# Kernel optimization log

Hardware: AMD Instinct MI355X
Metric: run time of the kernel (lower is better)

## Reference

```python
import jax, jax.numpy as jnp
import numpy as np

GAMMA = 1.0  # kernel_gamma

def setup_inputs() -> dict:
    key = jax.random.key(0)
    ks = jax.random.split(key, 8)
    B, T, D, P, H = 32, 512, 256, 512, 512
    return {
        "x": jax.random.normal(ks[0], (B, T, D), dtype=jnp.float32),
        "prototypes": jax.random.normal(ks[1], (P, D), dtype=jnp.float32),
        "W_lin": jax.random.normal(ks[2], (H, P), dtype=jnp.float32) * (1.0 / np.sqrt(P)),
        "b_lin": jax.random.normal(ks[3], (H,), dtype=jnp.float32) * 0.01,
        "W_ih": jax.random.normal(ks[4], (4 * H, H), dtype=jnp.float32) * (1.0 / np.sqrt(H)),
        "W_hh": jax.random.normal(ks[5], (4 * H, H), dtype=jnp.float32) * (1.0 / np.sqrt(H)),
        "b_ih": jax.random.normal(ks[6], (4 * H,), dtype=jnp.float32) * 0.01,
        "b_hh": jax.random.normal(ks[7], (4 * H,), dtype=jnp.float32) * 0.01,
    }

def _rbf(x_flat, prototypes):
    x2 = jnp.sum(x_flat * x_flat, axis=-1, keepdims=True)          # (N, 1)
    p2 = jnp.sum(prototypes * prototypes, axis=-1)                  # (P,)
    sq = x2 + p2[None, :] - 2.0 * (x_flat @ prototypes.T)           # (N, P)
    return jnp.exp(-GAMMA * jnp.maximum(sq, 0.0))

def _lstm(feats, W_ih, W_hh, b_ih, b_hh):
    # feats: (B, T, H); torch gate order i, f, g, o; zero initial state
    B, T, H = feats.shape
    xs = jnp.einsum('bth,gh->tbg', feats, W_ih) + (b_ih + b_hh)     # (T, B, 4H)

    def step(carry, x_t):
        h, c = carry
        gates = x_t + h @ W_hh.T                                     # (B, 4H)
        i, f, g, o = jnp.split(gates, 4, axis=-1)
        i, f, o = jax.nn.sigmoid(i), jax.nn.sigmoid(f), jax.nn.sigmoid(o)
        g = jnp.tanh(g)
        c = f * c + i * g
        h = o * jnp.tanh(c)
        return (h, c), h

    h0 = jnp.zeros((B, H), dtype=feats.dtype)
    c0 = jnp.zeros((B, H), dtype=feats.dtype)
    _, hs = jax.lax.scan(step, (h0, c0), xs)                         # hs: (T, B, H)
    return jnp.transpose(hs, (1, 0, 2))                              # (B, T, H)

def reference(x, prototypes, W_lin, b_lin, W_ih, W_hh, b_ih, b_hh):
    B, T, D = x.shape
    feats = _rbf(x.reshape(B * T, D), prototypes)                    # (B*T, P)
    feats = feats.reshape(B, T, -1) @ W_lin.T + b_lin                # (B, T, H)
    return _lstm(feats, W_ih, W_hh, b_ih, b_hh)
```

## Files before the change

kernel.cpp:

```cpp
#include <hip/hip_runtime.h>

#define Bb 32
#define Tt 512
#define Dd 256
#define Pp 512
#define Hh 512
#define G4 2048
#define TC 128
#define NG 8
#define WPG 16
#define NBG 4

__device__ __forceinline__ float sigmf(float x){ return 1.0f/(1.0f+__expf(-x)); }
__device__ __forceinline__ float tanhf_(float x){ return 1.0f - 2.0f/(__expf(2.0f*x)+1.0f); }

typedef __attribute__((ext_vector_type(8))) short v8s;
typedef __attribute__((ext_vector_type(4))) float f32x4;

__global__ void k_rowsq(const float* __restrict__ A, float* __restrict__ o, int M, int K){
  int m = blockIdx.x*blockDim.x + threadIdx.x;
  if (m >= M) return;
  const float4* a4 = (const float4*)(A + (size_t)m*K);
  float s = 0.f;
  for (int i = 0; i < K/4; ++i){ float4 v = a4[i]; s += v.x*v.x + v.y*v.y + v.z*v.z + v.w*v.w; }
  o[m] = s;
}

__global__ void k_transpose(const float* __restrict__ in, float* __restrict__ out, int M, int N){
  __shared__ float tile[32][33];
  int bn = blockIdx.x * 32;
  int bm = blockIdx.y * 32;
  int tx = threadIdx.x, ty = threadIdx.y;
  #pragma unroll
  for (int i = 0; i < 32; i += 8)
    tile[ty+i][tx] = in[(size_t)(bm+ty+i)*N + bn+tx];
  __syncthreads();
  #pragma unroll
  for (int i = 0; i < 32; i += 8)
    out[(size_t)(bn+ty+i)*M + bm+tx] = tile[tx][ty+i];
}

__global__ void k_bx(const float* __restrict__ Wih, const float* __restrict__ blin,
                     const float* __restrict__ bih, const float* __restrict__ bhh,
                     float* __restrict__ bx){
  int r = blockIdx.x*blockDim.x + threadIdx.x;
  const float4* w4 = (const float4*)(Wih + (size_t)r*Hh);
  const float4* b4 = (const float4*)blin;
  float s = 0.f;
  for (int i = 0; i < Hh/4; ++i){ float4 w=w4[i], b=b4[i]; s += w.x*b.x+w.y*b.y+w.z*b.z+w.w*b.w; }
  bx[r] = s + bih[r] + bhh[r];
}

__global__ void k_cvt_bf16(const float* __restrict__ in, ushort* __restrict__ out, int n4){
  int i = blockIdx.x*blockDim.x + threadIdx.x;
  if (i >= n4) return;
  float4 v = ((const float4*)in)[i];
  ushort4 o;
  uint u;
  u = __float_as_uint(v.x); u += 0x7FFF + ((u>>16)&1); o.x = (ushort)(u>>16);
  u = __float_as_uint(v.y); u += 0x7FFF + ((u>>16)&1); o.y = (ushort)(u>>16);
  u = __float_as_uint(v.z); u += 0x7FFF + ((u>>16)&1); o.z = (ushort)(u>>16);
  u = __float_as_uint(v.w); u += 0x7FFF + ((u>>16)&1); o.w = (ushort)(u>>16);
  ((ushort4*)out)[i] = o;
}

template<int EPI, bool REMAP>
__global__ __launch_bounds__(256) void k_gemm(const float* __restrict__ A, const float* __restrict__ Bm,
                                              float* __restrict__ C, int M, int N, int K,
                                              const float* __restrict__ rowAux,
                                              const float* __restrict__ colAux, int t0)
{
  __shared__ float As[16][132];
  __shared__ float Bs[16][68];
  const int tid = threadIdx.x;
  const int bm = blockIdx.x * 128;
  const int bn = blockIdx.y * 64;
  const int tm = (tid & 15) * 8;
  const int tn = (tid >> 4) * 4;
  const int arow = tid >> 1;
  const int akq  = (tid & 1) * 8;
  const int brow = tid >> 4;
  const int bcol = (tid & 15) * 4;
  const int am = bm + arow;
  const size_t aRow = REMAP ? ((size_t)(am >> 7) * Tt + t0 + (am & 127)) : (size_t)am;
  float acc[8][4] = {};
  for (int k0 = 0; k0 < K; k0 += 16){
    float4 a0 = *(const float4*)&A[aRow*K + k0 + akq];
    float4 a1 = *(const float4*)&A[aRow*K + k0 + akq + 4];
    float4 bv = *(const float4*)&Bm[(size_t)(k0 + brow)*N + bn + bcol];
    As[akq+0][arow]=a0.x; As[akq+1][arow]=a0.y; As[akq+2][arow]=a0.z; As[akq+3][arow]=a0.w;
    As[akq+4][arow]=a1.x; As[akq+5][arow]=a1.y; As[akq+6][arow]=a1.z; As[akq+7][arow]=a1.w;
    *(float4*)&Bs[brow][bcol] = bv;
    __syncthreads();
    #pragma unroll
    for (int kk = 0; kk < 16; ++kk){
      float4 x0 = *(const float4*)&As[kk][tm];
      float4 x1 = *(const float4*)&As[kk][tm+4];
      float4 y  = *(const float4*)&Bs[kk][tn];
      float av[8] = {x0.x,x0.y,x0.z,x0.w,x1.x,x1.y,x1.z,x1.w};
      #pragma unroll
      for (int i=0;i<8;++i){
        float a = av[i];
        acc[i][0] += a*y.x; acc[i][1] += a*y.y; acc[i][2] += a*y.z; acc[i][3] += a*y.w;
      }
    }
    __syncthreads();
  }
  #pragma unroll
  for (int i=0;i<8;++i){
    int m = bm + tm + i;
    size_t mAux = REMAP ? ((size_t)(m >> 7) * Tt + t0 + (m & 127)) : (size_t)m;
    float4 o;
    float vv[4];
    #pragma unroll
    for (int j=0;j<4;++j){
      int n = bn + tn + j;
      float v = acc[i][j];
      if (EPI==1) v = __expf(-fmaxf(rowAux[mAux] + colAux[n] - 2.f*v, 0.f));
      vv[j] = v;
    }
    o.x=vv[0]; o.y=vv[1]; o.z=vv[2]; o.w=vv[3];
    *(float4*)&C[(size_t)m*N + bn + tn] = o;
  }
}

__global__ __launch_bounds__(256) void k_xs_mfma(
    const ushort* __restrict__ A, const ushort* __restrict__ Bm,
    const float* __restrict__ bx, float* __restrict__ C, int M, int N, int K)
{
  __shared__ ushort As[128][72];
  __shared__ ushort Ws[128][72];
  const int tid  = threadIdx.x;
  const int bm   = blockIdx.x * 128;
  const int bn   = blockIdx.y * 128;
  const int lane = tid & 63;
  const int w    = tid >> 6;
  const int wr   = w >> 1, wc = w & 1;
  const int srow = tid >> 1;
  const int scol = (tid & 1) * 32;
  const int fr   = lane & 15;
  const int fk   = (lane >> 4) * 8;

  f32x4 acc[4][4] = {};

  for (int k0 = 0; k0 < K; k0 += 64){
    const ushort* ag = &A [(size_t)(bm + srow)*K + k0 + scol];
    const ushort* wg = &Bm[(size_t)(bn + srow)*K + k0 + scol];
    #pragma unroll
    for (int q = 0; q < 4; ++q){
      *(v8s*)&As[srow][scol + q*8] = *(const v8s*)&ag[q*8];
      *(v8s*)&Ws[srow][scol + q*8] = *(const v8s*)&wg[q*8];
    }
    __syncthreads();
    #pragma unroll
    for (int kk = 0; kk < 64; kk += 32){
      v8s af[4], bf[4];
      #pragma unroll
      for (int mi = 0; mi < 4; ++mi)
        af[mi] = *(const v8s*)&As[wr*64 + mi*16 + fr][kk + fk];
      #pragma unroll
      for (int ni = 0; ni < 4; ++ni)
        bf[ni] = *(const v8s*)&Ws[wc*64 + ni*16 + fr][kk + fk];
      #pragma unroll
      for (int mi = 0; mi < 4; ++mi)
        #pragma unroll
        for (int ni = 0; ni < 4; ++ni)
          acc[mi][ni] = __builtin_amdgcn_mfma_f32_16x16x32_bf16(af[mi], bf[ni], acc[mi][ni], 0, 0, 0);
    }
    __syncthreads();
  }

  const int cr = lane >> 4;
  #pragma unroll
  for (int ni = 0; ni < 4; ++ni){
    const int n = bn + wc*64 + ni*16 + fr;
    const float bb = bx[n];
    #pragma unroll
    for (int mi = 0; mi < 4; ++mi){
      #pragma unroll
      for (int r = 0; r < 4; ++r){
        const int m = bm + wr*64 + mi*16 + cr*4 + r;
        C[(size_t)m*N + n] = acc[mi][ni][r] + bb;
      }
    }
  }
}

__global__ __launch_bounds__(512, 2) void k_lstm_persist(
    const float* __restrict__ Whh, const float* __restrict__ xs,
    float* __restrict__ cbuf, float* __restrict__ out, int t0)
{
  __shared__ float hbuf[NBG*Hh];
  const int tid  = threadIdx.x;
  const int gid  = blockIdx.x & 7;
  const int wg   = blockIdx.x >> 3;
  const int gsel = tid & 3;
  const int ks   = (tid >> 2) & 15;
  const int ug   = tid >> 6;
  const int jbase = wg*32 + ug*4;

  float W[4][32];
  #pragma unroll
  for (int r = 0; r < 4; ++r){
    const float* wrow = &Whh[(size_t)(gsel*Hh + jbase + r)*Hh + ks*32];
    #pragma unroll
    for (int c = 0; c < 8; ++c){
      float4 w = *(const float4*)&wrow[c*4];
      W[r][c*4+0]=w.x; W[r][c*4+1]=w.y; W[r][c*4+2]=w.z; W[r][c*4+3]=w.w;
    }
  }

  const int rr = ks >> 2;
  const int bl = ks & 3;
  const int j  = jbase + rr;
  const int b  = gid*NBG + bl;
  float c_st = (t0 == 0) ? 0.f : cbuf[(size_t)b*Hh + j];

  const int sbl = tid >> 7;
  const int skb = (tid & 127) * 4;
  const int ssw = skb ^ (((skb >> 5) & 7) << 2);

  for (int tl = 0; tl < TC; ++tl){
    const int t = t0 + tl;
    float4 hv = {0.f,0.f,0.f,0.f};
    if (t > 0){
      const unsigned long long* src =
        (const unsigned long long*)&out[((size_t)(gid*NBG + sbl)*Tt + (t-1))*Hh + skb];
      unsigned long long a, c;
      for (;;){
        a = __hip_atomic_load(src+0, __ATOMIC_RELAXED, __HIP_MEMORY_SCOPE_AGENT);
        c = __hip_atomic_load(src+1, __ATOMIC_RELAXED, __HIP_MEMORY_SCOPE_AGENT);
        if ((unsigned)a != 0xFFFFFFFFu && (unsigned)(a>>32) != 0xFFFFFFFFu &&
            (unsigned)c != 0xFFFFFFFFu && (unsigned)(c>>32) != 0xFFFFFFFFu) break;
        __builtin_amdgcn_s_sleep(1);
      }
      hv.x = __uint_as_float((unsigned)a);
      hv.y = __uint_as_float((unsigned)(a>>32));
      hv.z = __uint_as_float((unsigned)c);
      hv.w = __uint_as_float((unsigned)(c>>32));
    }
    *(float4*)&hbuf[sbl*Hh + ssw] = hv;
    __syncthreads();

    float acc[4][4];
    #pragma unroll
    for (int r=0;r<4;++r){ acc[r][0]=0.f; acc[r][1]=0.f; acc[r][2]=0.f; acc[r][3]=0.f; }
    #pragma unroll
    for (int blq = 0; blq < 4; ++blq){
      const float* hb = &hbuf[blq*Hh + ks*32];
      #pragma unroll
      for (int c = 0; c < 8; ++c){
        float4 h4 = *(const float4*)&hb[(c*4) ^ ((ks & 7) << 2)];
        #pragma unroll
        for (int r = 0; r < 4; ++r){
          acc[r][blq] = fmaf(W[r][c*4+0], h4.x, acc[r][blq]);
          acc[r][blq] = fmaf(W[r][c*4+1], h4.y, acc[r][blq]);
          acc[r][blq] = fmaf(W[r][c*4+2], h4.z, acc[r][blq]);
          acc[r][blq] = fmaf(W[r][c*4+3], h4.w, acc[r][blq]);
        }
      }
    }

    #pragma unroll
    for (int m = 4; m <= 32; m <<= 1){
      #pragma unroll
      for (int r=0;r<4;++r){
        #pragma unroll
        for (int q=0;q<4;++q)
          acc[r][q] += __shfl_xor(acc[r][q], m, 64);
      }
    }
    float g = acc[0][0];
    #pragma unroll
    for (int r=0;r<4;++r){
      #pragma unroll
      for (int q=0;q<4;++q)
        if (ks == r*4+q) g = acc[r][q];
    }

    g += xs[((size_t)b*TC + tl)*G4 + gsel*Hh + j];
    const int lbase = (tid & 63) & ~3;
    float gi = __shfl(g, lbase+0, 64);
    float gf = __shfl(g, lbase+1, 64);
    float gg = __shfl(g, lbase+2, 64);
    float go = __shfl(g, lbase+3, 64);
    gi = sigmf(gi); gf = sigmf(gf); gg = tanhf_(gg); go = sigmf(go);
    c_st = gf*c_st + gi*gg;
    float h = go * tanhf_(c_st);
    if (gsel == 0)
      __hip_atomic_store(&out[((size_t)b*Tt + t)*Hh + j], h,
                         __ATOMIC_RELAXED, __HIP_MEMORY_SCOPE_AGENT);
  }
  if (gsel == 0) cbuf[(size_t)b*Hh + j] = c_st;
}

extern "C" void kernel_launch(void* const* d_in, const int* in_sizes, int n_in,
                              void* d_out, int out_size, void* d_ws, size_t ws_size,
                              hipStream_t stream)
{
  const float* x    = (const float*)d_in[0];
  const float* prot = (const float*)d_in[1];
  const float* Wlin = (const float*)d_in[2];
  const float* blin = (const float*)d_in[3];
  const float* Wih  = (const float*)d_in[4];
  const float* Whh  = (const float*)d_in[5];
  const float* bih  = (const float*)d_in[6];
  const float* bhh  = (const float*)d_in[7];
  float* out = (float*)d_out;
  float* ws  = (float*)d_ws;

  size_t off = 0;
  auto alloc = [&](size_t n)->float*{ float* p = ws + off; off += (n + 15) & ~((size_t)15); return p; };
  float* x2     = alloc((size_t)Bb*Tt);
  float* p2     = alloc(Pp);
  float* pT     = alloc((size_t)Dd*Pp);
  float* bx     = alloc(G4);
  float* Wx     = alloc((size_t)G4*Pp);
  ushort* WxB   = (ushort*)alloc((size_t)G4*Pp/2);
  float* cbuf   = alloc((size_t)Bb*Hh);
  float* featsC = alloc((size_t)Bb*TC*Pp);
  ushort* featsB= (ushort*)alloc((size_t)Bb*TC*Pp/2);
  float* xsC    = alloc((size_t)Bb*TC*G4);

  hipMemsetAsync(out, 0xFF, (size_t)Bb*Tt*Hh*sizeof(float), stream);

  k_rowsq<<<dim3((Bb*Tt)/256), dim3(256), 0, stream>>>(x, x2, Bb*Tt, Dd);
  k_rowsq<<<dim3(Pp/256), dim3(256), 0, stream>>>(prot, p2, Pp, Dd);
  k_transpose<<<dim3(Dd/32, Pp/32), dim3(32,8), 0, stream>>>(prot, pT, Pp, Dd);
  k_bx<<<dim3(G4/256), dim3(256), 0, stream>>>(Wih, blin, bih, bhh, bx);
  k_gemm<0,false><<<dim3(G4/128, Pp/64), dim3(256), 0, stream>>>(Wih, Wlin, Wx, G4, Pp, Hh, nullptr, nullptr, 0);
  k_cvt_bf16<<<dim3((G4*Pp/4)/256), dim3(256), 0, stream>>>(Wx, WxB, G4*Pp/4);

  for (int ch = 0; ch < Tt/TC; ++ch){
    int t0 = ch * TC;
    k_gemm<1,true><<<dim3((Bb*TC)/128, Pp/64), dim3(256), 0, stream>>>(
        x, pT, featsC, Bb*TC, Pp, Dd, x2, p2, t0);
    k_cvt_bf16<<<dim3((Bb*TC*Pp/4)/256), dim3(256), 0, stream>>>(featsC, featsB, Bb*TC*Pp/4);
    k_xs_mfma<<<dim3((Bb*TC)/128, G4/128), dim3(256), 0, stream>>>(
        featsB, WxB, bx, xsC, Bb*TC, G4, Pp);
    void* args[] = { (void*)&Whh, (void*)&xsC, (void*)&cbuf, (void*)&out, (void*)&t0 };
    hipLaunchCooperativeKernel((void*)k_lstm_persist, dim3(NG*WPG), dim3(512), args, 0, stream);
  }
}
```

Baseline: 3.432 ms.

## Repartition persistent LSTM kernel to one batch per workgroup with 1024 threads

```diff
diff --git a/kernel.cpp b/kernel.cpp
--- a/kernel.cpp
+++ b/kernel.cpp
@@ -7,9 +7,8 @@
 #define Hh 512
 #define G4 2048
 #define TC 128
-#define NG 8
-#define WPG 16
-#define NBG 4
+#define NG 32
+#define WPG 4
 
 __device__ __forceinline__ float sigmf(float x){ return 1.0f/(1.0f+__expf(-x)); }
 __device__ __forceinline__ float tanhf_(float x){ return 1.0f - 2.0f/(__expf(2.0f*x)+1.0f); }
@@ -186,22 +185,24 @@
   }
 }
 
-__global__ __launch_bounds__(512, 2) void k_lstm_persist(
-    const float* __restrict__ Whh, const float* __restrict__ xs,
-    float* __restrict__ cbuf, float* __restrict__ out, int t0)
+__global__ __launch_bounds__(1024) __attribute__((amdgpu_waves_per_eu(4, 4)))
+void k_lstm_persist(const float* __restrict__ Whh, const float* __restrict__ xs,
+                    float* __restrict__ cbuf, float* __restrict__ out, int t0)
 {
-  __shared__ float hbuf[NBG*Hh];
+  __shared__ float hbuf[Hh];
   const int tid  = threadIdx.x;
-  const int gid  = blockIdx.x & 7;
-  const int wg   = blockIdx.x >> 3;
+  const int lane = tid & 63;
   const int gsel = tid & 3;
   const int ks   = (tid >> 2) & 15;
   const int ug   = tid >> 6;
-  const int jbase = wg*32 + ug*4;
-
-  float W[4][32];
-  #pragma unroll
-  for (int r = 0; r < 4; ++r){
+  const int gid  = blockIdx.x & 31;
+  const int wg   = blockIdx.x >> 5;
+  const int jbase = wg*128 + ug*8;
+  const int b    = gid;
+
+  float W[8][32];
+  #pragma unroll
+  for (int r = 0; r < 8; ++r){
     const float* wrow = &Whh[(size_t)(gsel*Hh + jbase + r)*Hh + ks*32];
     #pragma unroll
     for (int c = 0; c < 8; ++c){
@@ -210,53 +211,52 @@
     }
   }
 
-  const int rr = ks >> 2;
-  const int bl = ks & 3;
-  const int j  = jbase + rr;
-  const int b  = gid*NBG + bl;
-  float c_st = (t0 == 0) ? 0.f : cbuf[(size_t)b*Hh + j];
-
-  const int sbl = tid >> 7;
+  const int jown = jbase + (ks & 7);
+  float c_st = (t0 == 0) ? 0.f : cbuf[(size_t)b*Hh + jown];
+
   const int skb = (tid & 127) * 4;
   const int ssw = skb ^ (((skb >> 5) & 7) << 2);
+  const bool stager = (tid < 128);
 
   for (int tl = 0; tl < TC; ++tl){
     const int t = t0 + tl;
-    float4 hv = {0.f,0.f,0.f,0.f};
-    if (t > 0){
-      const unsigned long long* src =
-        (const unsigned long long*)&out[((size_t)(gid*NBG + sbl)*Tt + (t-1))*Hh + skb];
-      unsigned long long a, c;
-      for (;;){
-        a = __hip_atomic_load(src+0, __ATOMIC_RELAXED, __HIP_MEMORY_SCOPE_AGENT);
-        c = __hip_atomic_load(src+1, __ATOMIC_RELAXED, __HIP_MEMORY_SCOPE_AGENT);
-        if ((unsigned)a != 0xFFFFFFFFu && (unsigned)(a>>32) != 0xFFFFFFFFu &&
-            (unsigned)c != 0xFFFFFFFFu && (unsigned)(c>>32) != 0xFFFFFFFFu) break;
-        __builtin_amdgcn_s_sleep(1);
+
+    if (stager){
+      float4 hv = {0.f,0.f,0.f,0.f};
+      if (t > 0){
+        const unsigned long long* src =
+          (const unsigned long long*)&out[((size_t)b*Tt + (t-1))*Hh + skb];
+        unsigned long long a, c;
+        for (;;){
+          a = __hip_atomic_load(src+0, __ATOMIC_RELAXED, __HIP_MEMORY_SCOPE_AGENT);
+          c = __hip_atomic_load(src+1, __ATOMIC_RELAXED, __HIP_MEMORY_SCOPE_AGENT);
+          if ((unsigned)a != 0xFFFFFFFFu && (unsigned)(a>>32) != 0xFFFFFFFFu &&
+              (unsigned)c != 0xFFFFFFFFu && (unsigned)(c>>32) != 0xFFFFFFFFu) break;
+          __builtin_amdgcn_s_sleep(1);
+        }
+        hv.x = __uint_as_float((unsigned)a);
+        hv.y = __uint_as_float((unsigned)(a>>32));
+        hv.z = __uint_as_float((unsigned)c);
+        hv.w = __uint_as_float((unsigned)(c>>32));
       }
-      hv.x = __uint_as_float((unsigned)a);
-      hv.y = __uint_as_float((unsigned)(a>>32));
-      hv.z = __uint_as_float((unsigned)c);
-      hv.w = __uint_as_float((unsigned)(c>>32));
-    }
-    *(float4*)&hbuf[sbl*Hh + ssw] = hv;
-    __syncthreads();
-
-    float acc[4][4];
-    #pragma unroll
-    for (int r=0;r<4;++r){ acc[r][0]=0.f; acc[r][1]=0.f; acc[r][2]=0.f; acc[r][3]=0.f; }
-    #pragma unroll
-    for (int blq = 0; blq < 4; ++blq){
-      const float* hb = &hbuf[blq*Hh + ks*32];
+      *(float4*)&hbuf[ssw] = hv;
+    }
+    __syncthreads();
+
+    float acc[8];
+    #pragma unroll
+    for (int r=0;r<8;++r) acc[r]=0.f;
+    {
+      const float* hb = &hbuf[ks*32];
       #pragma unroll
       for (int c = 0; c < 8; ++c){
         float4 h4 = *(const float4*)&hb[(c*4) ^ ((ks & 7) << 2)];
         #pragma unroll
-        for (int r = 0; r < 4; ++r){
-          acc[r][blq] = fmaf(W[r][c*4+0], h4.x, acc[r][blq]);
-          acc[r][blq] = fmaf(W[r][c*4+1], h4.y, acc[r][blq]);
-          acc[r][blq] = fmaf(W[r][c*4+2], h4.z, acc[r][blq]);
-          acc[r][blq] = fmaf(W[r][c*4+3], h4.w, acc[r][blq]);
+        for (int r = 0; r < 8; ++r){
+          acc[r] = fmaf(W[r][c*4+0], h4.x, acc[r]);
+          acc[r] = fmaf(W[r][c*4+1], h4.y, acc[r]);
+          acc[r] = fmaf(W[r][c*4+2], h4.z, acc[r]);
+          acc[r] = fmaf(W[r][c*4+3], h4.w, acc[r]);
         }
       }
     }
@@ -264,22 +264,16 @@
     #pragma unroll
     for (int m = 4; m <= 32; m <<= 1){
       #pragma unroll
-      for (int r=0;r<4;++r){
-        #pragma unroll
-        for (int q=0;q<4;++q)
-          acc[r][q] += __shfl_xor(acc[r][q], m, 64);
-      }
-    }
-    float g = acc[0][0];
-    #pragma unroll
-    for (int r=0;r<4;++r){
-      #pragma unroll
-      for (int q=0;q<4;++q)
-        if (ks == r*4+q) g = acc[r][q];
-    }
-
-    g += xs[((size_t)b*TC + tl)*G4 + gsel*Hh + j];
-    const int lbase = (tid & 63) & ~3;
+      for (int r=0;r<8;++r)
+        acc[r] += __shfl_xor(acc[r], m, 64);
+    }
+    float g = acc[0];
+    #pragma unroll
+    for (int r=1;r<8;++r)
+      if (ks == r) g = acc[r];
+
+    g += xs[((size_t)b*TC + tl)*G4 + gsel*Hh + jown];
+    const int lbase = lane & ~3;
     float gi = __shfl(g, lbase+0, 64);
     float gf = __shfl(g, lbase+1, 64);
     float gg = __shfl(g, lbase+2, 64);
@@ -287,11 +281,11 @@
     gi = sigmf(gi); gf = sigmf(gf); gg = tanhf_(gg); go = sigmf(go);
     c_st = gf*c_st + gi*gg;
     float h = go * tanhf_(c_st);
-    if (gsel == 0)
-      __hip_atomic_store(&out[((size_t)b*Tt + t)*Hh + j], h,
+    if (gsel == 0 && ks < 8)
+      __hip_atomic_store(&out[((size_t)b*Tt + t)*Hh + jown], h,
                          __ATOMIC_RELAXED, __HIP_MEMORY_SCOPE_AGENT);
   }
-  if (gsel == 0) cbuf[(size_t)b*Hh + j] = c_st;
+  if (gsel == 0 && ks < 8) cbuf[(size_t)b*Hh + jown] = c_st;
 }
 
 extern "C" void kernel_launch(void* const* d_in, const int* in_sizes, int n_in,
@@ -339,6 +333,6 @@
     k_xs_mfma<<<dim3((Bb*TC)/128, G4/128), dim3(256), 0, stream>>>(
         featsB, WxB, bx, xsC, Bb*TC, G4, Pp);
     void* args[] = { (void*)&Whh, (void*)&xsC, (void*)&cbuf, (void*)&out, (void*)&t0 };
-    hipLaunchCooperativeKernel((void*)k_lstm_persist, dim3(NG*WPG), dim3(512), args, 0, stream);
-  }
-}
+    hipLaunchCooperativeKernel((void*)k_lstm_persist, dim3(NG*WPG), dim3(1024), args, 0, stream);
+  }
+}
```

Result: slower. 11.16 ms (+225.1%).
